# Kernel tuning notes

Hardware: AMD Instinct MI355X
Metric: run time of the kernel (lower is better)

## Reference

```python
import jax, jax.numpy as jnp
import numpy as np

N_NODES = 50000
N_EDGES = 800000
NFEAT, NHID, NCLASS = 128, 256, 64


def setup_inputs() -> dict:
    key = jax.random.key(0)
    ks = jax.random.split(key, 8)
    x = jax.random.normal(ks[0], (N_NODES, NFEAT), dtype=jnp.float32)
    edge_index = jax.random.randint(ks[1], (2, N_EDGES), 0, N_NODES, dtype=jnp.int64)
    s1 = 1.0 / np.sqrt(NFEAT)
    s2 = 1.0 / np.sqrt(NHID)
    W1_neigh = jax.random.normal(ks[2], (NFEAT, NHID), dtype=jnp.float32) * s1
    W1_root = jax.random.normal(ks[3], (NFEAT, NHID), dtype=jnp.float32) * s1
    b1 = jnp.zeros((NHID,), dtype=jnp.float32)
    W2_neigh = jax.random.normal(ks[4], (NHID, NCLASS), dtype=jnp.float32) * s2
    W2_root = jax.random.normal(ks[5], (NHID, NCLASS), dtype=jnp.float32) * s2
    b2 = jnp.zeros((NCLASS,), dtype=jnp.float32)
    return {"x": x, "edge_index": edge_index, "W1_neigh": W1_neigh,
            "W1_root": W1_root, "b1": b1, "W2_neigh": W2_neigh,
            "W2_root": W2_root, "b2": b2}


def _sage_conv(h, src, dst, n_nodes, W_neigh, W_root, b):
    # mean aggregation of source features into destination nodes
    msg = h[src]                                                   # [E, d]
    summed = jax.ops.segment_sum(msg, dst, num_segments=n_nodes)   # [N, d]
    cnt = jax.ops.segment_sum(jnp.ones((src.shape[0],), h.dtype), dst,
                              num_segments=n_nodes)                # [N]
    mean = summed / jnp.maximum(cnt, 1.0)[:, None]
    return mean @ W_neigh + h @ W_root + b


def reference(x, edge_index, W1_neigh, W1_root, b1, W2_neigh, W2_root, b2):
    src, dst = edge_index[0], edge_index[1]
    n = x.shape[0]
    h = jax.nn.relu(_sage_conv(x, src, dst, n, W1_neigh, W1_root, b1))
    # dropout is identity in eval mode
    out = _sage_conv(h, src, dst, n, W2_neigh, W2_root, b2)
    return out
```

## Files before the change

### kernel.cpp

```cpp
#include <hip/hip_runtime.h>

#define N_NODES 50000
#define N_EDGES 800000
#define NFEAT   128
#define NHID    256
#define NCLASS  64

#define NPASS 8
#define PASS_W ((N_NODES + NPASS - 1) / NPASS)
#define ELLCAP 64

#define NPAIR   (N_EDGES / 2)
#define ECHUNK2 ((NPAIR + 255) / 256)
#define FILL_B  (ECHUNK2 * NPASS)
#define CVTX_B  ((N_NODES * 32 + 255) / 256)
#define CVTW_B  (((65536 + 32768) + 255) / 256)

typedef unsigned short u16;
typedef unsigned int   u32;
typedef __attribute__((ext_vector_type(8))) u16   u16x8;
typedef __attribute__((ext_vector_type(8))) short s16x8;
typedef __attribute__((ext_vector_type(4))) float f32x4;

__device__ inline u16 f2bf(float f) {
    u32 u = __float_as_uint(f);
    u32 r = (u + 0x7FFFu + ((u >> 16) & 1u)) >> 16;
    return (u16)r;
}
__device__ inline float bflo(u32 v) { return __uint_as_float(v << 16); }
__device__ inline float bfhi(u32 v) { return __uint_as_float(v & 0xFFFF0000u); }

#define GLOAD_LDS16(g, l)                                                        \
    __builtin_amdgcn_global_load_lds(                                            \
        (const __attribute__((address_space(1))) u32*)(const void*)(g),          \
        (__attribute__((address_space(3))) u32*)(void*)(l), 16, 0, 0)

__global__ __launch_bounds__(256) void prep_fill_kernel(const float* __restrict__ x,
                                                        const int* __restrict__ ei,
                                                        const float* __restrict__ W1r,
                                                        const float* __restrict__ W1n,
                                                        const float* __restrict__ W2n,
                                                        const float* __restrict__ W2r,
                                                        u16* __restrict__ xa,
                                                        int* __restrict__ cnt,
                                                        u16* __restrict__ ell,
                                                        u16* __restrict__ W1t,
                                                        u16* __restrict__ W2t) {
    int b = blockIdx.x;
    if (b < FILL_B) {
        int p = b & (NPASS - 1);
        int i = (b >> 3) * 256 + threadIdx.x;
        if (i >= NPAIR) return;
        int2 d2 = reinterpret_cast<const int2*>(ei + N_EDGES)[i];
        u32 lo = (u32)(p * PASS_W);
        bool in0 = ((u32)d2.x - lo) < (u32)PASS_W;
        bool in1 = ((u32)d2.y - lo) < (u32)PASS_W;
        if (in0 | in1) {
            int2 s2 = reinterpret_cast<const int2*>(ei)[i];
            if (in0) {
                int pos = atomicAdd(&cnt[d2.x], 1);
                if (pos < ELLCAP) ell[(size_t)d2.x * ELLCAP + pos] = (u16)s2.x;
            }
            if (in1) {
                int pos = atomicAdd(&cnt[d2.y], 1);
                if (pos < ELLCAP) ell[(size_t)d2.y * ELLCAP + pos] = (u16)s2.y;
            }
        }
    } else if (b < FILL_B + CVTX_B) {
        int idx = (b - FILL_B) * 256 + threadIdx.x;
        if (idx >= N_NODES * 32) return;
        int r  = idx >> 5;
        int c4 = (idx & 31) * 4;
        float4 v = *reinterpret_cast<const float4*>(x + (size_t)r * NFEAT + c4);
        uint2 o;
        o.x = (u32)f2bf(v.x) | ((u32)f2bf(v.y) << 16);
        o.y = (u32)f2bf(v.z) | ((u32)f2bf(v.w) << 16);
        *reinterpret_cast<uint2*>(xa + (size_t)r * 256 + c4) = o;
    } else {
        int id = (b - FILL_B - CVTX_B) * 256 + threadIdx.x;
        if (id < 65536) {
            int k = id & 255, n = id >> 8;
            float v = (k < NFEAT) ? W1r[(size_t)k * NHID + n]
                                  : W1n[(size_t)(k - NFEAT) * NHID + n];
            W1t[(size_t)n * 256 + k] = f2bf(v);
        } else if (id < 65536 + 32768) {
            int j = id - 65536;
            int k = j & 255, n = j >> 8;
            float v = (n < NCLASS) ? W2n[(size_t)k * NCLASS + n]
                                   : W2r[(size_t)k * NCLASS + (n - NCLASS)];
            W2t[(size_t)n * 256 + k] = f2bf(v);
        }
    }
}

__global__ __launch_bounds__(256) void gather1_kernel(const int* __restrict__ cnt,
                                                      const u16* __restrict__ ell,
                                                      u16* __restrict__ xa) {
    int gtid = blockIdx.x * 256 + threadIdx.x;
    int node = gtid >> 6;
    if (node >= N_NODES) return;
    int lane = threadIdx.x & 63;
    const u32* xrow = reinterpret_cast<const u32*>(xa);
    const u16* idx = ell + (size_t)node * ELLCAP;
    int deg = cnt[node];
    if (deg > ELLCAP) deg = ELLCAP;
    float ax = 0.0f, ay = 0.0f;
    int j = 0;
    for (; j + 16 <= deg; j += 16) {
        int s[16]; u32 v[16];
        #pragma unroll
        for (int q = 0; q < 16; ++q) s[q] = idx[j + q];
        #pragma unroll
        for (int q = 0; q < 16; ++q) v[q] = xrow[(size_t)s[q] * 128 + lane];
        #pragma unroll
        for (int q = 0; q < 16; ++q) { ax += bflo(v[q]); ay += bfhi(v[q]); }
    }
    for (; j + 8 <= deg; j += 8) {
        int s[8]; u32 v[8];
        #pragma unroll
        for (int q = 0; q < 8; ++q) s[q] = idx[j + q];
        #pragma unroll
        for (int q = 0; q < 8; ++q) v[q] = xrow[(size_t)s[q] * 128 + lane];
        #pragma unroll
        for (int q = 0; q < 8; ++q) { ax += bflo(v[q]); ay += bfhi(v[q]); }
    }
    for (; j < deg; ++j) {
        u32 v = xrow[(size_t)idx[j] * 128 + lane];
        ax += bflo(v);
        ay += bfhi(v);
    }
    float invd = 1.0f / fmaxf((float)deg, 1.0f);
    u32 packed = (u32)f2bf(ax * invd) | ((u32)f2bf(ay * invd) << 16);
    reinterpret_cast<u32*>(xa + (size_t)node * 256 + 128)[lane] = packed;
}

__global__ __launch_bounds__(256) void gather2_kernel(const int* __restrict__ cnt,
                                                      const u16* __restrict__ ell,
                                                      const u16* __restrict__ t,
                                                      float* __restrict__ out) {
    int gtid = blockIdx.x * 256 + threadIdx.x;
    int wave = gtid >> 6;
    int lane = threadIdx.x & 63;
    int node = wave * 2 + (lane >> 5);
    int l    = lane & 31;
    if (node >= N_NODES) return;
    const u32* trow = reinterpret_cast<const u32*>(t);
    const u16* idx = ell + (size_t)node * ELLCAP;
    int deg = cnt[node];
    if (deg > ELLCAP) deg = ELLCAP;
    float ax = 0.0f, ay = 0.0f;
    int j = 0;
    for (; j + 16 <= deg; j += 16) {
        int s[16]; u32 v[16];
        #pragma unroll
        for (int q = 0; q < 16; ++q) s[q] = idx[j + q];
        #pragma unroll
        for (int q = 0; q < 16; ++q) v[q] = trow[(size_t)s[q] * 32 + l];
        #pragma unroll
        for (int q = 0; q < 16; ++q) { ax += bflo(v[q]); ay += bfhi(v[q]); }
    }
    for (; j + 8 <= deg; j += 8) {
        int s[8]; u32 v[8];
        #pragma unroll
        for (int q = 0; q < 8; ++q) s[q] = idx[j + q];
        #pragma unroll
        for (int q = 0; q < 8; ++q) v[q] = trow[(size_t)s[q] * 32 + l];
        #pragma unroll
        for (int q = 0; q < 8; ++q) { ax += bflo(v[q]); ay += bfhi(v[q]); }
    }
    for (; j < deg; ++j) {
        u32 v = trow[(size_t)idx[j] * 32 + l];
        ax += bflo(v); ay += bfhi(v);
    }
    float invd = 1.0f / fmaxf((float)deg, 1.0f);
    float* o = out + (size_t)node * NCLASS + l * 2;
    o[0] += ax * invd;
    o[1] += ay * invd;
}

__global__ __launch_bounds__(256) void gemm1_mfma(const u16* __restrict__ xa,
                                                  const u16* __restrict__ W1t,
                                                  const float* __restrict__ b1,
                                                  u16* __restrict__ h) {
    __shared__ u16 As[128 * 32];
    __shared__ u16 Bs[128 * 32];
    const int tid = threadIdx.x;
    const int r0 = blockIdx.x * 128;
    const int n0 = blockIdx.y * 128;
    const int wid = tid >> 6, ln = tid & 63;
    const int wm = (wid & 1) * 64, wn = (wid >> 1) * 64;
    const int lr = ln & 15;
    const int lq = ln >> 4;

    f32x4 acc[4][4] = {};

    for (int k0 = 0; k0 < 256; k0 += 32) {
        #pragma unroll
        for (int it = 0; it < 2; ++it) {
            int c   = it * 256 + tid;
            int row = c >> 2;
            int ko  = (c & 3) * 8;
            GLOAD_LDS16(xa  + (size_t)(r0 + row) * 256 + k0 + ko, As + c * 8);
            GLOAD_LDS16(W1t + (size_t)(n0 + row) * 256 + k0 + ko, Bs + c * 8);
        }
        __syncthreads();

        s16x8 af[4], bf[4];
        #pragma unroll
        for (int i = 0; i < 4; ++i)
            af[i] = *reinterpret_cast<const s16x8*>(As + (wm + i * 16 + lr) * 32 + lq * 8);
        #pragma unroll
        for (int j = 0; j < 4; ++j)
            bf[j] = *reinterpret_cast<const s16x8*>(Bs + (wn + j * 16 + lr) * 32 + lq * 8);
        #pragma unroll
        for (int i = 0; i < 4; ++i)
            #pragma unroll
            for (int j = 0; j < 4; ++j)
                acc[i][j] = __builtin_amdgcn_mfma_f32_16x16x32_bf16(af[i], bf[j], acc[i][j], 0, 0, 0);
        __syncthreads();
    }

    #pragma unroll
    for (int i = 0; i < 4; ++i) {
        #pragma unroll
        for (int j = 0; j < 4; ++j) {
            int col = n0 + wn + j * 16 + lr;
            float bias = b1[col];
            #pragma unroll
            for (int r = 0; r < 4; ++r) {
                int row = r0 + wm + i * 16 + lq * 4 + r;
                if (row < N_NODES)
                    h[(size_t)row * 256 + col] = f2bf(fmaxf(acc[i][j][r] + bias, 0.0f));
            }
        }
    }
}

__global__ __launch_bounds__(256) void gemm2_mfma(const u16* __restrict__ h,
                                                  const u16* __restrict__ W2t,
                                                  const float* __restrict__ b2,
                                                  u16* __restrict__ t,
                                                  float* __restrict__ out) {
    __shared__ u16 As[128 * 32];
    __shared__ u16 Bs[128 * 32];
    const int tid = threadIdx.x;
    const int r0 = blockIdx.x * 128;
    const int wid = tid >> 6, ln = tid & 63;
    const int wm = (wid & 1) * 64, wn = (wid >> 1) * 64;
    const int lr = ln & 15;
    const int lq = ln >> 4;

    f32x4 acc[4][4] = {};

    for (int k0 = 0; k0 < 256; k0 += 32) {
        #pragma unroll
        for (int it = 0; it < 2; ++it) {
            int c   = it * 256 + tid;
            int row = c >> 2;
            int ko  = (c & 3) * 8;
            GLOAD_LDS16(h   + (size_t)(r0 + row) * 256 + k0 + ko, As + c * 8);
            GLOAD_LDS16(W2t + (size_t)row * 256 + k0 + ko,        Bs + c * 8);
        }
        __syncthreads();

        s16x8 af[4], bf[4];
        #pragma unroll
        for (int i = 0; i < 4; ++i)
            af[i] = *reinterpret_cast<const s16x8*>(As + (wm + i * 16 + lr) * 32 + lq * 8);
        #pragma unroll
        for (int j = 0; j < 4; ++j)
            bf[j] = *reinterpret_cast<const s16x8*>(Bs + (wn + j * 16 + lr) * 32 + lq * 8);
        #pragma unroll
        for (int i = 0; i < 4; ++i)
            #pragma unroll
            for (int j = 0; j < 4; ++j)
                acc[i][j] = __builtin_amdgcn_mfma_f32_16x16x32_bf16(af[i], bf[j], acc[i][j], 0, 0, 0);
        __syncthreads();
    }

    #pragma unroll
    for (int i = 0; i < 4; ++i) {
        #pragma unroll
        for (int j = 0; j < 4; ++j) {
            int col = wn + j * 16 + lr;
            #pragma unroll
            for (int r = 0; r < 4; ++r) {
                int row = r0 + wm + i * 16 + lq * 4 + r;
                if (row >= N_NODES) continue;
                if (col < NCLASS) {
                    t[(size_t)row * NCLASS + col] = f2bf(acc[i][j][r]);
                } else {
                    int c = col - NCLASS;
                    out[(size_t)row * NCLASS + c] = acc[i][j][r] + b2[c];
                }
            }
        }
    }
}

extern "C" void kernel_launch(void* const* d_in, const int* in_sizes, int n_in,
                              void* d_out, int out_size, void* d_ws, size_t ws_size,
                              hipStream_t stream) {
    const float* x    = (const float*)d_in[0];
    const int*   ei   = (const int*)d_in[1];
    const float* W1n  = (const float*)d_in[2];
    const float* W1r  = (const float*)d_in[3];
    const float* b1   = (const float*)d_in[4];
    const float* W2n  = (const float*)d_in[5];
    const float* W2r  = (const float*)d_in[6];
    const float* b2   = (const float*)d_in[7];
    float* out = (float*)d_out;

    int* cnt = (int*)d_ws;
    u16* ell = (u16*)(cnt + 50048);
    u16* xa  = ell + (size_t)N_NODES * ELLCAP;
    u16* h   = xa + (size_t)N_NODES * 256;
    u16* t   = h  + (size_t)N_NODES * 256;
    u16* W1t = t  + (size_t)N_NODES * 64;
    u16* W2t = W1t + 65536;

    hipMemsetAsync(cnt, 0, 50048 * sizeof(int), stream);

    prep_fill_kernel<<<FILL_B + CVTX_B + CVTW_B, 256, 0, stream>>>(
        x, ei, W1r, W1n, W2n, W2r, xa, cnt, ell, W1t, W2t);

    gather1_kernel<<<(N_NODES * 64 + 255) / 256, 256, 0, stream>>>(cnt, ell, xa);
    gemm1_mfma<<<dim3((N_NODES + 127) / 128, 2), 256, 0, stream>>>(xa, W1t, b1, h);

    gemm2_mfma<<<(N_NODES + 127) / 128, 256, 0, stream>>>(h, W2t, b2, t, out);
    gather2_kernel<<<(N_NODES * 32 + 255) / 256, 256, 0, stream>>>(cnt, ell, t, out);
}
```

Measured before the change: 227.4 us.

## Build ELL adjacency via two-level bucket binning with shared-memory atomics

Replaces the 8-pass global-atomic ELL fill with a two-stage build. Edges are first binned into 56 coarse destination buckets using block-local histograms and one global atomic per bucket. A second kernel then scans each bucket per 128-node tile and fills ELL slots with LDS atomics, writing the counts directly. This cuts global atomic traffic and the repeated edge reads, at the cost of an extra kernel launch, a bucket staging buffer, and a fixed bucket capacity that could overflow on skewed inputs.

```diff
diff --git a/kernel.cpp b/kernel.cpp
--- a/kernel.cpp
+++ b/kernel.cpp
@@ -6,19 +6,21 @@
 #define NHID    256
 #define NCLASS  64
 
-#define NPASS 8
-#define PASS_W ((N_NODES + NPASS - 1) / NPASS)
-#define ELLCAP 64
-
-#define NPAIR   (N_EDGES / 2)
-#define ECHUNK2 ((NPAIR + 255) / 256)
-#define FILL_B  (ECHUNK2 * NPASS)
+#define ELLCAP  64
+
+#define NBUCK   56
+#define BWIDTH  896
+#define BCAP    16384
+#define BIN_CH  4096
+#define BIN_B   ((N_EDGES + BIN_CH - 1) / BIN_CH)
+#define NFINE   ((N_NODES + 127) / 128)
+#define FPB     7
+
 #define CVTX_B  ((N_NODES * 32 + 255) / 256)
 #define CVTW_B  (((65536 + 32768) + 255) / 256)
 
 typedef unsigned short u16;
 typedef unsigned int   u32;
-typedef __attribute__((ext_vector_type(8))) u16   u16x8;
 typedef __attribute__((ext_vector_type(8))) short s16x8;
 typedef __attribute__((ext_vector_type(4))) float f32x4;
 
@@ -35,39 +37,51 @@
         (const __attribute__((address_space(1))) u32*)(const void*)(g),          \
         (__attribute__((address_space(3))) u32*)(void*)(l), 16, 0, 0)
 
-__global__ __launch_bounds__(256) void prep_fill_kernel(const float* __restrict__ x,
-                                                        const int* __restrict__ ei,
-                                                        const float* __restrict__ W1r,
-                                                        const float* __restrict__ W1n,
-                                                        const float* __restrict__ W2n,
-                                                        const float* __restrict__ W2r,
-                                                        u16* __restrict__ xa,
-                                                        int* __restrict__ cnt,
-                                                        u16* __restrict__ ell,
-                                                        u16* __restrict__ W1t,
-                                                        u16* __restrict__ W2t) {
+__global__ __launch_bounds__(256) void prep_kernel(const float* __restrict__ x,
+                                                   const int* __restrict__ ei,
+                                                   const float* __restrict__ W1r,
+                                                   const float* __restrict__ W1n,
+                                                   const float* __restrict__ W2n,
+                                                   const float* __restrict__ W2r,
+                                                   u16* __restrict__ xa,
+                                                   u32* __restrict__ gcnt,
+                                                   u32* __restrict__ bbuf,
+                                                   u16* __restrict__ W1t,
+                                                   u16* __restrict__ W2t) {
     int b = blockIdx.x;
-    if (b < FILL_B) {
-        int p = b & (NPASS - 1);
-        int i = (b >> 3) * 256 + threadIdx.x;
-        if (i >= NPAIR) return;
-        int2 d2 = reinterpret_cast<const int2*>(ei + N_EDGES)[i];
-        u32 lo = (u32)(p * PASS_W);
-        bool in0 = ((u32)d2.x - lo) < (u32)PASS_W;
-        bool in1 = ((u32)d2.y - lo) < (u32)PASS_W;
-        if (in0 | in1) {
-            int2 s2 = reinterpret_cast<const int2*>(ei)[i];
-            if (in0) {
-                int pos = atomicAdd(&cnt[d2.x], 1);
-                if (pos < ELLCAP) ell[(size_t)d2.x * ELLCAP + pos] = (u16)s2.x;
+    if (b < BIN_B) {
+        __shared__ u32 hist[NBUCK];
+        __shared__ u32 base[NBUCK];
+        int tid = threadIdx.x;
+        if (tid < NBUCK) hist[tid] = 0;
+        __syncthreads();
+        u32 ek[16]; u32 rk[16]; int bk[16];
+        int i0 = b * BIN_CH;
+        #pragma unroll
+        for (int k = 0; k < 16; ++k) {
+            int i = i0 + k * 256 + tid;
+            bk[k] = -1;
+            if (i < N_EDGES) {
+                u32 s = (u32)ei[i];
+                u32 d = (u32)ei[N_EDGES + i];
+                int bu = (int)(d / BWIDTH);
+                ek[k] = (d << 16) | s;
+                bk[k] = bu;
+                rk[k] = atomicAdd(&hist[bu], 1u);
             }
-            if (in1) {
-                int pos = atomicAdd(&cnt[d2.y], 1);
-                if (pos < ELLCAP) ell[(size_t)d2.y * ELLCAP + pos] = (u16)s2.y;
+        }
+        __syncthreads();
+        if (tid < NBUCK) base[tid] = atomicAdd(&gcnt[tid], hist[tid]);
+        __syncthreads();
+        #pragma unroll
+        for (int k = 0; k < 16; ++k) {
+            if (bk[k] >= 0) {
+                u32 pos = base[bk[k]] + rk[k];
+                if (pos < BCAP) bbuf[((u32)bk[k] << 14) + pos] = ek[k];
             }
         }
-    } else if (b < FILL_B + CVTX_B) {
-        int idx = (b - FILL_B) * 256 + threadIdx.x;
+    } else if (b < BIN_B + CVTX_B) {
+        int idx = (b - BIN_B) * 256 + threadIdx.x;
         if (idx >= N_NODES * 32) return;
         int r  = idx >> 5;
         int c4 = (idx & 31) * 4;
@@ -77,7 +91,7 @@
         o.y = (u32)f2bf(v.z) | ((u32)f2bf(v.w) << 16);
         *reinterpret_cast<uint2*>(xa + (size_t)r * 256 + c4) = o;
     } else {
-        int id = (b - FILL_B - CVTX_B) * 256 + threadIdx.x;
+        int id = (b - BIN_B - CVTX_B) * 256 + threadIdx.x;
         if (id < 65536) {
             int k = id & 255, n = id >> 8;
             float v = (k < NFEAT) ? W1r[(size_t)k * NHID + n]
@@ -91,6 +105,38 @@
             W2t[(size_t)n * 256 + k] = f2bf(v);
         }
     }
+}
+
+__global__ __launch_bounds__(512) void ell_build_kernel(const u32* __restrict__ bbuf,
+                                                        const u32* __restrict__ gcnt,
+                                                        int* __restrict__ cnt,
+                                                        u16* __restrict__ ell) {
+    __shared__ u32 hist[128];
+    int tid = threadIdx.x;
+    int f   = blockIdx.x;
+    int cb  = f / FPB;
+    int n0  = f * 128;
+    if (tid < 128) hist[tid] = 0;
+    __syncthreads();
+    int m = (int)gcnt[cb]; if (m > BCAP) m = BCAP;
+    const u32* bk = bbuf + ((u32)cb << 14);
+    int i = tid;
+    for (; i + 1536 < m; i += 2048) {
+        u32 e0 = bk[i], e1 = bk[i + 512], e2 = bk[i + 1024], e3 = bk[i + 1536];
+        u32 d0 = (e0 >> 16) - (u32)n0, d1 = (e1 >> 16) - (u32)n0;
+        u32 d2 = (e2 >> 16) - (u32)n0, d3 = (e3 >> 16) - (u32)n0;
+        if (d0 < 128u) { u32 p = atomicAdd(&hist[d0], 1u); if (p < ELLCAP) ell[(size_t)(n0 + (int)d0) * ELLCAP + p] = (u16)e0; }
+        if (d1 < 128u) { u32 p = atomicAdd(&hist[d1], 1u); if (p < ELLCAP) ell[(size_t)(n0 + (int)d1) * ELLCAP + p] = (u16)e1; }
+        if (d2 < 128u) { u32 p = atomicAdd(&hist[d2], 1u); if (p < ELLCAP) ell[(size_t)(n0 + (int)d2) * ELLCAP + p] = (u16)e2; }
+        if (d3 < 128u) { u32 p = atomicAdd(&hist[d3], 1u); if (p < ELLCAP) ell[(size_t)(n0 + (int)d3) * ELLCAP + p] = (u16)e3; }
+    }
+    for (; i < m; i += 512) {
+        u32 e = bk[i];
+        u32 d = (e >> 16) - (u32)n0;
+        if (d < 128u) { u32 p = atomicAdd(&hist[d], 1u); if (p < ELLCAP) ell[(size_t)(n0 + (int)d) * ELLCAP + p] = (u16)e; }
+    }
+    __syncthreads();
+    if (tid < 128) cnt[n0 + tid] = (int)hist[tid];
 }
 
 __global__ __launch_bounds__(256) void gather1_kernel(const int* __restrict__ cnt,
@@ -311,18 +357,21 @@
     const float* b2   = (const float*)d_in[7];
     float* out = (float*)d_out;
 
-    int* cnt = (int*)d_ws;
-    u16* ell = (u16*)(cnt + 50048);
-    u16* xa  = ell + (size_t)N_NODES * ELLCAP;
-    u16* h   = xa + (size_t)N_NODES * 256;
-    u16* t   = h  + (size_t)N_NODES * 256;
-    u16* W1t = t  + (size_t)N_NODES * 64;
-    u16* W2t = W1t + 65536;
-
-    hipMemsetAsync(cnt, 0, 50048 * sizeof(int), stream);
-
-    prep_fill_kernel<<<FILL_B + CVTX_B + CVTW_B, 256, 0, stream>>>(
-        x, ei, W1r, W1n, W2n, W2r, xa, cnt, ell, W1t, W2t);
+    u32* gcnt = (u32*)d_ws;
+    u32* bbuf = gcnt + 64;
+    int* cnt  = (int*)(bbuf + ((size_t)NBUCK << 14));
+    u16* ell  = (u16*)(cnt + 50048);
+    u16* xa   = ell + (size_t)N_NODES * ELLCAP;
+    u16* h    = xa + (size_t)N_NODES * 256;
+    u16* t    = h  + (size_t)N_NODES * 256;
+    u16* W1t  = t  + (size_t)N_NODES * 64;
+    u16* W2t  = W1t + 65536;
+
+    hipMemsetAsync(gcnt, 0, 64 * sizeof(u32), stream);
+
+    prep_kernel<<<BIN_B + CVTX_B + CVTW_B, 256, 0, stream>>>(
+        x, ei, W1r, W1n, W2n, W2r, xa, gcnt, bbuf, W1t, W2t);
+    ell_build_kernel<<<NFINE, 512, 0, stream>>>(bbuf, gcnt, cnt, ell);
 
     gather1_kernel<<<(N_NODES * 64 + 255) / 256, 256, 0, stream>>>(cnt, ell, xa);
     gemm1_mfma<<<dim3((N_NODES + 127) / 128, 2), 256, 0, stream>>>(xa, W1t, b1, h);
```

After: 209.1 us. -8.1%, faster.
